# Kernel tuning notes

Measured on AMD Instinct MI355X. Metric: run time of the kernel, lower is better.

Reference implementation:

```python
import jax, jax.numpy as jnp
import numpy as np

GAMMA_1 = 4.0
GAMMA_2 = 5.0
EPS = 1e-8  # torch CosineSimilarity default eps

B, D, T, N = 64, 256, 24, 289


def setup_inputs() -> dict:
    key = jax.random.key(0)
    k1, k2 = jax.random.split(key)
    e = jax.random.normal(k1, (B, D, T), dtype=jnp.float32)  # word embeddings [B, D, T]
    v = jax.random.normal(k2, (B, D, N), dtype=jnp.float32)  # region features [B, D, N]
    return {"e": e, "v": v}


def _pair_scores(e, v):
    # Vectorized all-pairs version of batch_score(e[i], v[j]) -> S[i, j]
    # s = e[i].T @ v[j] : [B, B, T, N]
    s = jnp.einsum('idt,jdn->ijtn', e, v)
    s_norm = jax.nn.softmax(s, axis=3)               # softmax over regions (dim=1)
    alpha = jax.nn.softmax(GAMMA_1 * s_norm, axis=2)  # softmax over words (dim=0)
    # c[t, d] = sum_n alpha[t, n] * v[d, n]  -> [B, B, T, D]
    c = jnp.einsum('ijtn,jdn->ijtd', alpha, v)
    # CosineSimilarity(dim=1)(c.t() [D,T], e [D,T]) -> cosine over the T axis, shape [D]
    dot = jnp.einsum('ijtd,idt->ijd', c, e)           # [B, B, D]
    c_norm = jnp.sqrt(jnp.sum(c * c, axis=2))         # [B, B, D]
    e_norm = jnp.sqrt(jnp.sum(e * e, axis=2))         # [B, D]
    R = dot / jnp.maximum(c_norm * e_norm[:, None, :], EPS)
    # log(exp(g2 * R).sum(dim=0)) ** (1/g2), logsumexp over D
    return jnp.power(jax.nn.logsumexp(GAMMA_2 * R, axis=2), 1.0 / GAMMA_2)  # [B, B]


def reference(e, v):
    S = _pair_scores(e, v)          # S[i, j] = batch_score(e[i], v[j])
    batch_sum_score_d = S.sum(axis=1)  # sum_j S[i, j]
    batch_sum_score_q = S.sum(axis=0)  # sum_j S[j, i]
    return (batch_sum_score_d, batch_sum_score_q)
```

## Files before the change

### kernel.cpp

```cpp
#include <hip/hip_runtime.h>
#include <hip/hip_bf16.h>
#include <math.h>

#define BB 64
#define DD 256
#define TT 24
#define NR 289

typedef float f32x4  __attribute__((ext_vector_type(4)));
typedef float f32x16 __attribute__((ext_vector_type(16)));
typedef short bf16x8 __attribute__((ext_vector_type(8)));

#define ETF_OFF  0ul
#define VTF_OFF  1048576ul
#define VB2_OFF  11534336ul
#define EE_OFF   22020096ul
#define SMAT_OFF 23592960ul

__global__ __launch_bounds__(256) void conv_kernel(const float* __restrict__ e,
                                                   const float* __restrict__ v,
                                                   __hip_bfloat16* __restrict__ eTf,
                                                   float* __restrict__ eE,
                                                   __hip_bfloat16* __restrict__ vTf,
                                                   __hip_bfloat16* __restrict__ vbf2) {
    __shared__ float ld[32][321];
    int tid = threadIdx.x;

    if (blockIdx.x >= 512) {
        int i = blockIdx.x - 512;
        const float* ei = e + (size_t)i * DD * TT;
        bf16x8* dst = (bf16x8*)eTf + (size_t)i * 1024;
        #pragma unroll
        for (int p = 0; p < 4; ++p) {
            int idx = tid + p * 256;
            int r = idx & 31, sidx = idx >> 5;
            int d0 = sidx * 8;
            __hip_bfloat16 tmp[8];
            #pragma unroll
            for (int q = 0; q < 8; ++q) {
                float f = (r < TT) ? ei[(d0 + q) * TT + r] : 0.f;
                tmp[q] = __float2bfloat16(f);
            }
            dst[idx] = *(bf16x8*)tmp;
        }
        float* dstE = eE + (size_t)i * 6144;
        #pragma unroll
        for (int p = 0; p < 24; ++p) {
            int idx = tid + p * 256;
            int r = idx & 31, rest = idx >> 5;
            int reg = rest % 12, gdt = rest / 12;
            int g2 = gdt & 1, dt = gdt >> 1;
            int t = (reg & 3) + 8 * (reg >> 2) + 4 * g2;
            dstE[idx] = ei[(dt * 32 + r) * TT + t];
        }
        return;
    }

    int j = blockIdx.x >> 3;
    int dbase = (blockIdx.x & 7) * 32;
    const float* vj = v + (size_t)j * DD * NR;
    for (int r = 0; r < 32; ++r) {
        const float* row = vj + (size_t)(dbase + r) * NR;
        ld[r][tid] = row[tid];
        if (tid < 64) {
            int n = 256 + tid;
            ld[r][n] = (n < NR) ? row[n] : 0.f;
        }
    }
    __syncthreads();
    {
        bf16x8* dT = (bf16x8*)vTf + (size_t)j * 10240;
        #pragma unroll
        for (int p = 0; p < 5; ++p) {
            int idx = tid + p * 256;
            int r = idx & 31, rest = idx >> 5;
            int nt = rest % 10, sl = rest / 10;
            int sidx = (dbase >> 3) + sl;
            __hip_bfloat16 tmp[8];
            #pragma unroll
            for (int q = 0; q < 8; ++q)
                tmp[q] = __float2bfloat16(ld[sl * 8 + q][nt * 32 + r]);
            dT[(nt * 32 + sidx) * 32 + r] = *(bf16x8*)tmp;
        }
    }
    {
        bf16x8* dB = (bf16x8*)vbf2 + (size_t)j * 10240;
        int dt = dbase >> 5;
        #pragma unroll
        for (int p = 0; p < 5; ++p) {
            int idx = tid + p * 256;
            int r = idx & 31, ks = idx >> 5;
            __hip_bfloat16 tmp[8];
            #pragma unroll
            for (int q = 0; q < 8; ++q)
                tmp[q] = __float2bfloat16(ld[r][ks * 8 + q]);
            dB[(dt * 40 + ks) * 32 + r] = *(bf16x8*)tmp;
        }
    }
}

__global__ __launch_bounds__(256, 6) void pair_kernel(const __hip_bfloat16* __restrict__ eTf,
                                                      const __hip_bfloat16* __restrict__ vTf,
                                                      const __hip_bfloat16* __restrict__ vbf2,
                                                      const float* __restrict__ eE,
                                                      float* __restrict__ Smat) {
    __shared__ __align__(16) __hip_bfloat16 alpha[32 * 320];

    const int tid = threadIdx.x;
    const int wave = tid >> 6, lane = tid & 63;
    const int r = lane & 31, g2 = lane >> 5;
    const int bid = (blockIdx.x & 7) * 512 + (blockIdx.x >> 3);
    const int i = bid & 63, j = bid >> 6;

    char* ab = (char*)alpha;

    {
        uint32_t* rz = (uint32_t*)(ab + 24 * 640);
        #pragma unroll
        for (int q = 0; q < 5; ++q) rz[tid + q * 256] = 0u;
        int t = tid >> 3, n0 = 304 + 2 * (tid & 7);
        int boff = (t * 640 + 2 * n0) ^ ((t & 7) << 4);
        *(uint32_t*)(ab + boff) = 0u;
    }

    const bf16x8* eF = (const bf16x8*)eTf + (size_t)i * 1024;
    const bf16x8* vF = (const bf16x8*)vTf + (size_t)j * 10240;
    #pragma unroll
    for (int ti = 0; ti < 3; ++ti) {
        int nt2 = wave + ti * 4;
        if (nt2 < 10) {
            f32x16 acc;
            #pragma unroll
            for (int z = 0; z < 16; ++z) acc[z] = 0.f;
            int n = nt2 * 32 + r;
            #pragma unroll
            for (int s = 0; s < 16; ++s) {
                bf16x8 af = eF[(s * 2 + g2) * 32 + r];
                bf16x8 bf = vF[(nt2 * 32 + s * 2 + g2) * 32 + r];
                acc = __builtin_amdgcn_mfma_f32_32x32x16_bf16(af, bf, acc, 0, 0, 0);
            }
            if (nt2 < 9 || r < 16) {
                #pragma unroll
                for (int reg = 0; reg < 12; ++reg) {
                    int t = (reg & 3) + 8 * (reg >> 2) + 4 * g2;
                    int boff = (t * 640 + 2 * n) ^ ((t & 7) << 4);
                    *(__hip_bfloat16*)(ab + boff) = __float2bfloat16(acc[reg]);
                }
            }
        }
    }
    __syncthreads();

    #pragma unroll
    for (int tt = 0; tt < 6; ++tt) {
        int t = wave * 6 + tt;
        int base = t * 640, sw = (t & 7) << 4;
        float vls[5];
        #pragma unroll
        for (int k5 = 0; k5 < 5; ++k5) {
            int n = k5 * 64 + lane;
            vls[k5] = (n < NR)
                ? __bfloat162float(*(const __hip_bfloat16*)(ab + ((base + 2 * n) ^ sw)))
                : -INFINITY;
        }
        float m = vls[0];
        #pragma unroll
        for (int k5 = 1; k5 < 5; ++k5) m = fmaxf(m, vls[k5]);
        #pragma unroll
        for (int mk = 32; mk >= 1; mk >>= 1) m = fmaxf(m, __shfl_xor(m, mk, 64));
        float sum = 0.f;
        #pragma unroll
        for (int k5 = 0; k5 < 5; ++k5) { vls[k5] = __expf(vls[k5] - m); sum += vls[k5]; }
        #pragma unroll
        for (int mk = 32; mk >= 1; mk >>= 1) sum += __shfl_xor(sum, mk, 64);
        float inv = 1.f / sum;
        #pragma unroll
        for (int k5 = 0; k5 < 5; ++k5) {
            int n = k5 * 64 + lane;
            if (n < NR)
                *(__hip_bfloat16*)(ab + ((base + 2 * n) ^ sw)) = __float2bfloat16(vls[k5] * inv);
        }
    }
    __syncthreads();

    for (int p = 0; p < 2; ++p) {
        int n = p * 256 + tid;
        if (n < NR) {
            float vals[TT];
            #pragma unroll
            for (int t = 0; t < TT; ++t)
                vals[t] = __bfloat162float(
                    *(const __hip_bfloat16*)(ab + ((t * 640 + 2 * n) ^ ((t & 7) << 4))));
            float m = vals[0];
            #pragma unroll
            for (int t = 1; t < TT; ++t) m = fmaxf(m, vals[t]);
            m *= 4.0f;
            float sum = 0.f;
            #pragma unroll
            for (int t = 0; t < TT; ++t) { vals[t] = __expf(4.0f * vals[t] - m); sum += vals[t]; }
            float inv = 1.f / sum;
            #pragma unroll
            for (int t = 0; t < TT; ++t)
                *(__hip_bfloat16*)(ab + ((t * 640 + 2 * n) ^ ((t & 7) << 4))) =
                    __float2bfloat16(vals[t] * inv);
        }
    }
    __syncthreads();

    const bf16x8* vB2f = (const bf16x8*)vbf2 + (size_t)j * 10240;
    const float* eEp = eE + (size_t)i * 6144;

    float ssum = 0.f;
    #pragma unroll
    for (int ti2 = 0; ti2 < 2; ++ti2) {
        int dt = wave + ti2 * 4;
        f32x16 acc;
        #pragma unroll
        for (int z = 0; z < 16; ++z) acc[z] = 0.f;
        int sw = (r & 7) << 4;
        #pragma unroll
        for (int ks = 0; ks < 20; ++ks) {
            bf16x8 af = *(const bf16x8*)(ab + ((r * 640 + ks * 32 + g2 * 16) ^ sw));
            bf16x8 bf = vB2f[(dt * 40 + ks * 2 + g2) * 32 + r];
            acc = __builtin_amdgcn_mfma_f32_32x32x16_bf16(af, bf, acc, 0, 0, 0);
        }
        float dot = 0.f, cn2 = 0.f, en2 = 0.f;
        #pragma unroll
        for (int reg = 0; reg < 12; ++reg) {
            float ev = eEp[((dt * 2 + g2) * 12 + reg) * 32 + r];
            dot = fmaf(acc[reg], ev, dot);
            cn2 = fmaf(acc[reg], acc[reg], cn2);
            en2 = fmaf(ev, ev, en2);
        }
        dot += __shfl_xor(dot, 32, 64);
        cn2 += __shfl_xor(cn2, 32, 64);
        en2 += __shfl_xor(en2, 32, 64);
        float R = dot / fmaxf(sqrtf(cn2) * sqrtf(en2), 1e-8f);
        ssum += __expf(5.f * R);
    }
    #pragma unroll
    for (int mk = 1; mk <= 32; mk <<= 1) ssum += __shfl_xor(ssum, mk, 64);
    __syncthreads();
    float* red = (float*)alpha;
    if (lane == 0) red[wave] = ssum;
    __syncthreads();
    if (tid == 0) {
        float total = red[0] + red[1] + red[2] + red[3];
        float lse = logf(total * 0.5f);
        Smat[bid] = powf(lse, 0.2f);
    }
}

__global__ void reduce_kernel(const float* __restrict__ Smat, float* __restrict__ out) {
    int k = threadIdx.x;
    float s = 0.f;
    if (k < 64) {
        int i = k;
        for (int j = 0; j < BB; ++j) s += Smat[j * 64 + i];
        out[i] = s;
    } else {
        int jq = k - 64;
        for (int i = 0; i < BB; ++i) s += Smat[jq * 64 + i];
        out[64 + jq] = s;
    }
}

extern "C" void kernel_launch(void* const* d_in, const int* in_sizes, int n_in,
                              void* d_out, int out_size, void* d_ws, size_t ws_size,
                              hipStream_t stream) {
    const float* e = (const float*)d_in[0];
    const float* v = (const float*)d_in[1];
    float* out = (float*)d_out;
    char* ws = (char*)d_ws;
    __hip_bfloat16* eTf  = (__hip_bfloat16*)(ws + ETF_OFF);
    __hip_bfloat16* vTf  = (__hip_bfloat16*)(ws + VTF_OFF);
    __hip_bfloat16* vbf2 = (__hip_bfloat16*)(ws + VB2_OFF);
    float* eE  = (float*)(ws + EE_OFF);
    float* Smat = (float*)(ws + SMAT_OFF);

    conv_kernel<<<576, 256, 0, stream>>>(e, v, eTf, eE, vTf, vbf2);
    pair_kernel<<<BB * BB, 256, 0, stream>>>(eTf, vTf, vbf2, eE, Smat);
    reduce_kernel<<<1, 128, 0, stream>>>(Smat, out);
}
```

Baseline: 104.3 us.

## Process two e-batches per block to reuse v fragments across pairs

After: 124.1 us. 1.19x slower.

```diff
diff --git a/kernel.cpp b/kernel.cpp
--- a/kernel.cpp
+++ b/kernel.cpp
@@ -99,22 +99,23 @@
     }
 }
 
-__global__ __launch_bounds__(256, 6) void pair_kernel(const __hip_bfloat16* __restrict__ eTf,
+__global__ __launch_bounds__(256, 4) void pair_kernel(const __hip_bfloat16* __restrict__ eTf,
                                                       const __hip_bfloat16* __restrict__ vTf,
                                                       const __hip_bfloat16* __restrict__ vbf2,
                                                       const float* __restrict__ eE,
                                                       float* __restrict__ Smat) {
-    __shared__ __align__(16) __hip_bfloat16 alpha[32 * 320];
+    __shared__ __align__(16) __hip_bfloat16 alpha[2][32 * 320];
 
     const int tid = threadIdx.x;
     const int wave = tid >> 6, lane = tid & 63;
     const int r = lane & 31, g2 = lane >> 5;
-    const int bid = (blockIdx.x & 7) * 512 + (blockIdx.x >> 3);
-    const int i = bid & 63, j = bid >> 6;
-
-    char* ab = (char*)alpha;
-
-    {
+    const int bid = (blockIdx.x & 7) * 256 + (blockIdx.x >> 3);
+    const int j = bid >> 5;
+    const int i0 = (bid & 31) * 2, i1 = i0 + 1;
+
+    #pragma unroll
+    for (int b = 0; b < 2; ++b) {
+        char* ab = (char*)alpha[b];
         uint32_t* rz = (uint32_t*)(ab + 24 * 640);
         #pragma unroll
         for (int q = 0; q < 5; ++q) rz[tid + q * 256] = 0u;
@@ -123,28 +124,32 @@
         *(uint32_t*)(ab + boff) = 0u;
     }
 
-    const bf16x8* eF = (const bf16x8*)eTf + (size_t)i * 1024;
-    const bf16x8* vF = (const bf16x8*)vTf + (size_t)j * 10240;
+    const bf16x8* eF0 = (const bf16x8*)eTf + (size_t)i0 * 1024;
+    const bf16x8* eF1 = (const bf16x8*)eTf + (size_t)i1 * 1024;
+    const bf16x8* vF  = (const bf16x8*)vTf + (size_t)j * 10240;
+    char* ab0 = (char*)alpha[0];
+    char* ab1 = (char*)alpha[1];
     #pragma unroll
     for (int ti = 0; ti < 3; ++ti) {
         int nt2 = wave + ti * 4;
         if (nt2 < 10) {
-            f32x16 acc;
-            #pragma unroll
-            for (int z = 0; z < 16; ++z) acc[z] = 0.f;
+            f32x16 a0, a1;
+            #pragma unroll
+            for (int z = 0; z < 16; ++z) { a0[z] = 0.f; a1[z] = 0.f; }
             int n = nt2 * 32 + r;
             #pragma unroll
             for (int s = 0; s < 16; ++s) {
-                bf16x8 af = eF[(s * 2 + g2) * 32 + r];
                 bf16x8 bf = vF[(nt2 * 32 + s * 2 + g2) * 32 + r];
-                acc = __builtin_amdgcn_mfma_f32_32x32x16_bf16(af, bf, acc, 0, 0, 0);
+                a0 = __builtin_amdgcn_mfma_f32_32x32x16_bf16(eF0[(s * 2 + g2) * 32 + r], bf, a0, 0, 0, 0);
+                a1 = __builtin_amdgcn_mfma_f32_32x32x16_bf16(eF1[(s * 2 + g2) * 32 + r], bf, a1, 0, 0, 0);
             }
             if (nt2 < 9 || r < 16) {
                 #pragma unroll
                 for (int reg = 0; reg < 12; ++reg) {
                     int t = (reg & 3) + 8 * (reg >> 2) + 4 * g2;
                     int boff = (t * 640 + 2 * n) ^ ((t & 7) << 4);
-                    *(__hip_bfloat16*)(ab + boff) = __float2bfloat16(acc[reg]);
+                    *(__hip_bfloat16*)(ab0 + boff) = __float2bfloat16(a0[reg]);
+                    *(__hip_bfloat16*)(ab1 + boff) = __float2bfloat16(a1[reg]);
                 }
             }
         }
@@ -152,102 +157,116 @@
     __syncthreads();
 
     #pragma unroll
-    for (int tt = 0; tt < 6; ++tt) {
-        int t = wave * 6 + tt;
-        int base = t * 640, sw = (t & 7) << 4;
-        float vls[5];
-        #pragma unroll
-        for (int k5 = 0; k5 < 5; ++k5) {
-            int n = k5 * 64 + lane;
-            vls[k5] = (n < NR)
-                ? __bfloat162float(*(const __hip_bfloat16*)(ab + ((base + 2 * n) ^ sw)))
-                : -INFINITY;
-        }
-        float m = vls[0];
-        #pragma unroll
-        for (int k5 = 1; k5 < 5; ++k5) m = fmaxf(m, vls[k5]);
-        #pragma unroll
-        for (int mk = 32; mk >= 1; mk >>= 1) m = fmaxf(m, __shfl_xor(m, mk, 64));
-        float sum = 0.f;
-        #pragma unroll
-        for (int k5 = 0; k5 < 5; ++k5) { vls[k5] = __expf(vls[k5] - m); sum += vls[k5]; }
-        #pragma unroll
-        for (int mk = 32; mk >= 1; mk >>= 1) sum += __shfl_xor(sum, mk, 64);
-        float inv = 1.f / sum;
-        #pragma unroll
-        for (int k5 = 0; k5 < 5; ++k5) {
-            int n = k5 * 64 + lane;
-            if (n < NR)
-                *(__hip_bfloat16*)(ab + ((base + 2 * n) ^ sw)) = __float2bfloat16(vls[k5] * inv);
-        }
-    }
-    __syncthreads();
-
-    for (int p = 0; p < 2; ++p) {
-        int n = p * 256 + tid;
-        if (n < NR) {
-            float vals[TT];
-            #pragma unroll
-            for (int t = 0; t < TT; ++t)
-                vals[t] = __bfloat162float(
-                    *(const __hip_bfloat16*)(ab + ((t * 640 + 2 * n) ^ ((t & 7) << 4))));
-            float m = vals[0];
-            #pragma unroll
-            for (int t = 1; t < TT; ++t) m = fmaxf(m, vals[t]);
-            m *= 4.0f;
+    for (int b = 0; b < 2; ++b) {
+        char* ab = (char*)alpha[b];
+        #pragma unroll
+        for (int tt = 0; tt < 6; ++tt) {
+            int t = wave * 6 + tt;
+            int base = t * 640, sw = (t & 7) << 4;
+            float vls[5];
+            #pragma unroll
+            for (int k5 = 0; k5 < 5; ++k5) {
+                int n = k5 * 64 + lane;
+                vls[k5] = (n < NR)
+                    ? __bfloat162float(*(const __hip_bfloat16*)(ab + ((base + 2 * n) ^ sw)))
+                    : -INFINITY;
+            }
+            float m = vls[0];
+            #pragma unroll
+            for (int k5 = 1; k5 < 5; ++k5) m = fmaxf(m, vls[k5]);
+            #pragma unroll
+            for (int mk = 32; mk >= 1; mk >>= 1) m = fmaxf(m, __shfl_xor(m, mk, 64));
             float sum = 0.f;
             #pragma unroll
-            for (int t = 0; t < TT; ++t) { vals[t] = __expf(4.0f * vals[t] - m); sum += vals[t]; }
+            for (int k5 = 0; k5 < 5; ++k5) { vls[k5] = __expf(vls[k5] - m); sum += vls[k5]; }
+            #pragma unroll
+            for (int mk = 32; mk >= 1; mk >>= 1) sum += __shfl_xor(sum, mk, 64);
             float inv = 1.f / sum;
             #pragma unroll
-            for (int t = 0; t < TT; ++t)
-                *(__hip_bfloat16*)(ab + ((t * 640 + 2 * n) ^ ((t & 7) << 4))) =
-                    __float2bfloat16(vals[t] * inv);
+            for (int k5 = 0; k5 < 5; ++k5) {
+                int n = k5 * 64 + lane;
+                if (n < NR)
+                    *(__hip_bfloat16*)(ab + ((base + 2 * n) ^ sw)) = __float2bfloat16(vls[k5] * inv);
+            }
+        }
+    }
+    __syncthreads();
+
+    #pragma unroll
+    for (int b = 0; b < 2; ++b) {
+        char* ab = (char*)alpha[b];
+        for (int p = 0; p < 2; ++p) {
+            int n = p * 256 + tid;
+            if (n < NR) {
+                float vals[TT];
+                #pragma unroll
+                for (int t = 0; t < TT; ++t)
+                    vals[t] = __bfloat162float(
+                        *(const __hip_bfloat16*)(ab + ((t * 640 + 2 * n) ^ ((t & 7) << 4))));
+                float m = vals[0];
+                #pragma unroll
+                for (int t = 1; t < TT; ++t) m = fmaxf(m, vals[t]);
+                m *= 4.0f;
+                float sum = 0.f;
+                #pragma unroll
+                for (int t = 0; t < TT; ++t) { vals[t] = __expf(4.0f * vals[t] - m); sum += vals[t]; }
+                float inv = 1.f / sum;
+                #pragma unroll
+                for (int t = 0; t < TT; ++t)
+                    *(__hip_bfloat16*)(ab + ((t * 640 + 2 * n) ^ ((t & 7) << 4))) =
+                        __float2bfloat16(vals[t] * inv);
+            }
         }
     }
     __syncthreads();
 
     const bf16x8* vB2f = (const bf16x8*)vbf2 + (size_t)j * 10240;
-    const float* eEp = eE + (size_t)i * 6144;
-
-    float ssum = 0.f;
+    const float* eE0 = eE + (size_t)i0 * 6144;
+    const float* eE1 = eE + (size_t)i1 * 6144;
+
+    float ss0 = 0.f, ss1 = 0.f;
     #pragma unroll
     for (int ti2 = 0; ti2 < 2; ++ti2) {
         int dt = wave + ti2 * 4;
-        f32x16 acc;
-        #pragma unroll
-        for (int z = 0; z < 16; ++z) acc[z] = 0.f;
+        f32x16 a0, a1;
+        #pragma unroll
+        for (int z = 0; z < 16; ++z) { a0[z] = 0.f; a1[z] = 0.f; }
         int sw = (r & 7) << 4;
         #pragma unroll
         for (int ks = 0; ks < 20; ++ks) {
-            bf16x8 af = *(const bf16x8*)(ab + ((r * 640 + ks * 32 + g2 * 16) ^ sw));
             bf16x8 bf = vB2f[(dt * 40 + ks * 2 + g2) * 32 + r];
-            acc = __builtin_amdgcn_mfma_f32_32x32x16_bf16(af, bf, acc, 0, 0, 0);
-        }
-        float dot = 0.f, cn2 = 0.f, en2 = 0.f;
+            int boff = (r * 640 + ks * 32 + g2 * 16) ^ sw;
+            bf16x8 af0 = *(const bf16x8*)(ab0 + boff);
+            bf16x8 af1 = *(const bf16x8*)(ab1 + boff);
+            a0 = __builtin_amdgcn_mfma_f32_32x32x16_bf16(af0, bf, a0, 0, 0, 0);
+            a1 = __builtin_amdgcn_mfma_f32_32x32x16_bf16(af1, bf, a1, 0, 0, 0);
+        }
+        float d0 = 0.f, c0 = 0.f, e0 = 0.f, d1 = 0.f, c1 = 0.f, e1 = 0.f;
         #pragma unroll
         for (int reg = 0; reg < 12; ++reg) {
-            float ev = eEp[((dt * 2 + g2) * 12 + reg) * 32 + r];
-            dot = fmaf(acc[reg], ev, dot);
-            cn2 = fmaf(acc[reg], acc[reg], cn2);
-            en2 = fmaf(ev, ev, en2);
-        }
-        dot += __shfl_xor(dot, 32, 64);
-        cn2 += __shfl_xor(cn2, 32, 64);
-        en2 += __shfl_xor(en2, 32, 64);
-        float R = dot / fmaxf(sqrtf(cn2) * sqrtf(en2), 1e-8f);
-        ssum += __expf(5.f * R);
-    }
-    #pragma unroll
-    for (int mk = 1; mk <= 32; mk <<= 1) ssum += __shfl_xor(ssum, mk, 64);
-    __syncthreads();
-    float* red = (float*)alpha;
-    if (lane == 0) red[wave] = ssum;
+            int off = ((dt * 2 + g2) * 12 + reg) * 32 + r;
+            float ev0 = eE0[off], ev1 = eE1[off];
+            d0 = fmaf(a0[reg], ev0, d0); c0 = fmaf(a0[reg], a0[reg], c0); e0 = fmaf(ev0, ev0, e0);
+            d1 = fmaf(a1[reg], ev1, d1); c1 = fmaf(a1[reg], a1[reg], c1); e1 = fmaf(ev1, ev1, e1);
+        }
+        d0 += __shfl_xor(d0, 32, 64); c0 += __shfl_xor(c0, 32, 64); e0 += __shfl_xor(e0, 32, 64);
+        d1 += __shfl_xor(d1, 32, 64); c1 += __shfl_xor(c1, 32, 64); e1 += __shfl_xor(e1, 32, 64);
+        float R0 = d0 / fmaxf(sqrtf(c0) * sqrtf(e0), 1e-8f);
+        float R1 = d1 / fmaxf(sqrtf(c1) * sqrtf(e1), 1e-8f);
+        ss0 += __expf(5.f * R0);
+        ss1 += __expf(5.f * R1);
+    }
+    #pragma unroll
+    for (int mk = 1; mk <= 32; mk <<= 1) { ss0 += __shfl_xor(ss0, mk, 64); ss1 += __shfl_xor(ss1, mk, 64); }
+    __syncthreads();
+    float* red = (float*)alpha[0];
+    if (lane == 0) { red[wave] = ss0; red[4 + wave] = ss1; }
     __syncthreads();
     if (tid == 0) {
-        float total = red[0] + red[1] + red[2] + red[3];
-        float lse = logf(total * 0.5f);
-        Smat[bid] = powf(lse, 0.2f);
+        float t0 = red[0] + red[1] + red[2] + red[3];
+        float t1 = red[4] + red[5] + red[6] + red[7];
+        Smat[j * 64 + i0] = powf(logf(t0 * 0.5f), 0.2f);
+        Smat[j * 64 + i1] = powf(logf(t1 * 0.5f), 0.2f);
     }
 }
 
@@ -279,6 +298,6 @@
     float* Smat = (float*)(ws + SMAT_OFF);
 
     conv_kernel<<<576, 256, 0, stream>>>(e, v, eTf, eE, vTf, vbf2);
-    pair_kernel<<<BB * BB, 256, 0, stream>>>(eTf, vTf, vbf2, eE, Smat);
+    pair_kernel<<<2048, 256, 0, stream>>>(eTf, vTf, vbf2, eE, Smat);
     reduce_kernel<<<1, 128, 0, stream>>>(Smat, out);
 }
```
